# Kernel tuning notes

Measured on AMD Instinct MI355X. Metric: run time of the kernel, lower is better.

Reference implementation:

```python
import jax, jax.numpy as jnp
import numpy as np

B, V = 8, 128  # batch, cubic volume side


def setup_inputs() -> dict:
    key = jax.random.key(0)
    k1, k2 = jax.random.split(key)
    input_volume1 = jax.random.normal(k1, (B, V, V, V), dtype=jnp.float32)
    input_volume2 = jax.random.normal(k2, (B, V, V, V), dtype=jnp.float32)
    return {"input_volume1": input_volume1, "input_volume2": input_volume2}


def reference(input_volume1, input_volume2):
    # Full circular 3D cross-correlation over all relative shifts:
    #   out[b, t] = sum_r v1[b, r] * v2[b, (r + t) mod V]  (t, r are 3D indices)
    # computed via the convolution theorem with real FFTs.
    axes = (1, 2, 3)
    f1 = jnp.fft.rfftn(input_volume1, axes=axes)          # [B, V, V, V//2+1] complex
    f2 = jnp.fft.rfftn(input_volume2, axes=axes)
    out = jnp.fft.irfftn(f1 * jnp.conj(f2), s=(V, V, V), axes=axes)
    return out.astype(jnp.float32)
```

## Files before the change

kernel.cpp:

```cpp
#include <hip/hip_runtime.h>
#include <math.h>


#define V    128
#define V2   16384
#define V3   2097152
#define NB   8
#define PR1  134
#define PC1  66
#define P3Q  130
#define PH3  34
#define SLICE (V * PH3)

__device__ __forceinline__ int bitrev7(int x) {
  return (int)(__brev((unsigned)x) >> 25);
}
__device__ __forceinline__ int negrev(int j) {
  int k = bitrev7(j);
  return bitrev7((V - k) & (V - 1));
}

__device__ __forceinline__ float2 cmul(float2 a, float2 b) {
  return make_float2(a.x * b.x - a.y * b.y, a.x * b.y + a.y * b.x);
}
__device__ __forceinline__ float2 cmulc(float2 a, float2 b) {
  return make_float2(a.x * b.x + a.y * b.y, a.y * b.x - a.x * b.y);
}
__device__ __forceinline__ float2 csqr(float2 a) {
  return make_float2(a.x * a.x - a.y * a.y, 2.0f * a.x * a.y);
}
__device__ __forceinline__ float2 f2add(float2 a, float2 b) {
  return make_float2(a.x + b.x, a.y + b.y);
}
__device__ __forceinline__ float2 f2sub(float2 a, float2 b) {
  return make_float2(a.x - b.x, a.y - b.y);
}
__device__ __forceinline__ float2 NI(float2 z) { return make_float2(z.y, -z.x); }
__device__ __forceinline__ float2 PI(float2 z) { return make_float2(-z.y, z.x); }

#define KC1 0.92387953251128675613f
#define KS1 0.38268343236508977173f
#define KR  0.70710678118654752440f

template <int CTRL>
__device__ __forceinline__ float dppf(float v) {
  return __int_as_float(
      __builtin_amdgcn_update_dpp(0, __float_as_int(v), CTRL, 0xF, 0xF, true));
}
template <int CTRL>
__device__ __forceinline__ float2 dpp2(float2 v) {
  return make_float2(dppf<CTRL>(v.x), dppf<CTRL>(v.y));
}

struct WFT {
  float2 w1, w2, w4, w8, ts4, ts2;
  float sg4, sg2, sg1;
  bool up4, up2;
  int e;

  __device__ void init(int lq) {
    e = lq ^ (((lq >> 2) & 1) * 3);
    const float k = -6.28318530717958647692f / 128.0f;
    w1 = make_float2(cosf(k * (float)e), sinf(k * (float)e));
    w2 = csqr(w1);
    w4 = csqr(w2);
    w8 = csqr(w4);
    up4 = (e >> 2) & 1;
    up2 = (e >> 1) & 1;
    const bool up1 = e & 1;
    sg4 = up4 ? -1.0f : 1.0f;
    sg2 = up2 ? -1.0f : 1.0f;
    sg1 = up1 ? -1.0f : 1.0f;
    const int m4 = e & 3;
    float2 w8p = (m4 == 0) ? make_float2(1.0f, 0.0f)
               : (m4 == 1) ? make_float2(KR, -KR)
               : (m4 == 2) ? make_float2(0.0f, -1.0f)
                           : make_float2(-KR, -KR);
    ts4 = up4 ? w8p : make_float2(1.0f, 0.0f);
    ts2 = (up2 && (e & 1)) ? make_float2(0.0f, -1.0f) : make_float2(1.0f, 0.0f);
  }

  __device__ __forceinline__ void xf4(float2* c, int n) const {
#pragma unroll
    for (int j = 0; j < n; ++j) {
      float2 p = dpp2<0x141>(c[j]);
      float2 t = make_float2(fmaf(c[j].x, sg4, p.x), fmaf(c[j].y, sg4, p.y));
      c[j] = cmul(t, ts4);
    }
#pragma unroll
    for (int j = 0; j < n; ++j) {
      float2 p = dpp2<0x4E>(c[j]);
      float2 t = make_float2(fmaf(c[j].x, sg2, p.x), fmaf(c[j].y, sg2, p.y));
      c[j] = cmul(t, ts2);
    }
#pragma unroll
    for (int j = 0; j < n; ++j) {
      float2 p = dpp2<0xB1>(c[j]);
      c[j] = make_float2(fmaf(c[j].x, sg1, p.x), fmaf(c[j].y, sg1, p.y));
    }
  }
  __device__ __forceinline__ void xi4(float2* c, int n) const {
#pragma unroll
    for (int j = 0; j < n; ++j) {
      float2 p = dpp2<0xB1>(c[j]);
      c[j] = make_float2(fmaf(c[j].x, sg1, p.x), fmaf(c[j].y, sg1, p.y));
    }
#pragma unroll
    for (int j = 0; j < n; ++j) {
      float2 m = cmulc(c[j], ts2);
      float2 q = make_float2(up2 ? m.x : c[j].x, up2 ? m.y : c[j].y);
      float2 p = dpp2<0x4E>(q);
      c[j] = make_float2(fmaf(q.x, sg2, p.x), fmaf(q.y, sg2, p.y));
    }
#pragma unroll
    for (int j = 0; j < n; ++j) {
      float2 m = cmulc(c[j], ts4);
      float2 q = make_float2(up4 ? m.x : c[j].x, up4 ? m.y : c[j].y);
      float2 p = dpp2<0x141>(q);
      c[j] = make_float2(fmaf(q.x, sg4, p.x), fmaf(q.y, sg4, p.y));
    }
  }

  __device__ __forceinline__ void fwd128(float2 c[16]) const {
    const float2 tA = cmul(w1, make_float2(KC1, -KS1));
    const float2 tB = cmul(w1, make_float2(KR, -KR));
    const float2 tC = cmul(w1, make_float2(KS1, -KC1));
#pragma unroll
    for (int j = 0; j < 8; ++j) {
      float2 u = c[j], v = c[j + 8];
      c[j] = f2add(u, v);
      const int q = j & 3;
      float2 tw = (q == 0) ? w1 : (q == 1) ? tA : (q == 2) ? tB : tC;
      float2 t = cmul(f2sub(u, v), tw);
      c[j + 8] = (j < 4) ? t : NI(t);
    }
    const float2 t2 = cmul(w2, make_float2(KR, -KR));
#pragma unroll
    for (int g = 0; g < 2; ++g) {
#pragma unroll
      for (int j0 = 0; j0 < 4; ++j0) {
        const int j = g * 8 + j0;
        float2 u = c[j], v = c[j + 4];
        c[j] = f2add(u, v);
        float2 t = cmul(f2sub(u, v), (j0 & 1) ? t2 : w2);
        c[j + 4] = (j0 < 2) ? t : NI(t);
      }
    }
    const float2 w4n = NI(w4);
#pragma unroll
    for (int g = 0; g < 4; ++g) {
#pragma unroll
      for (int j0 = 0; j0 < 2; ++j0) {
        const int j = g * 4 + j0;
        float2 u = c[j], v = c[j + 2];
        c[j] = f2add(u, v);
        c[j + 2] = cmul(f2sub(u, v), j0 ? w4n : w4);
      }
    }
#pragma unroll
    for (int j = 0; j < 16; j += 2) {
      float2 u = c[j], v = c[j + 1];
      c[j] = f2add(u, v);
      c[j + 1] = cmul(f2sub(u, v), w8);
    }
    xf4(c, 16);
  }

  __device__ __forceinline__ void inv128(float2 c[16]) const {
    xi4(c, 16);
#pragma unroll
    for (int j = 0; j < 16; j += 2) {
      float2 m = cmulc(c[j + 1], w8);
      float2 u = c[j];
      c[j] = f2add(u, m);
      c[j + 1] = f2sub(u, m);
    }
#pragma unroll
    for (int g = 0; g < 4; ++g) {
#pragma unroll
      for (int j0 = 0; j0 < 2; ++j0) {
        const int j = g * 4 + j0;
        float2 m0 = cmulc(c[j + 2], w4);
        float2 m = j0 ? PI(m0) : m0;
        float2 u = c[j];
        c[j] = f2add(u, m);
        c[j + 2] = f2sub(u, m);
      }
    }
    const float2 t2 = cmul(w2, make_float2(KR, -KR));
#pragma unroll
    for (int g = 0; g < 2; ++g) {
#pragma unroll
      for (int j0 = 0; j0 < 4; ++j0) {
        const int j = g * 8 + j0;
        float2 m0 = cmulc(c[j + 4], (j0 & 1) ? t2 : w2);
        float2 m = (j0 < 2) ? m0 : PI(m0);
        float2 u = c[j];
        c[j] = f2add(u, m);
        c[j + 4] = f2sub(u, m);
      }
    }
    const float2 tA = cmul(w1, make_float2(KC1, -KS1));
    const float2 tB = cmul(w1, make_float2(KR, -KR));
    const float2 tC = cmul(w1, make_float2(KS1, -KC1));
#pragma unroll
    for (int j = 0; j < 8; ++j) {
      const int q = j & 3;
      float2 tw = (q == 0) ? w1 : (q == 1) ? tA : (q == 2) ? tB : tC;
      float2 m0 = cmulc(c[j + 8], tw);
      float2 m = (j < 4) ? m0 : PI(m0);
      float2 u = c[j];
      c[j] = f2add(u, m);
      c[j + 8] = f2sub(u, m);
    }
  }

  __device__ __forceinline__ void fwd64(float2 c[8]) const {
    const float2 t2 = cmul(w2, make_float2(KR, -KR));
#pragma unroll
    for (int j = 0; j < 4; ++j) {
      float2 u = c[j], v = c[j + 4];
      c[j] = f2add(u, v);
      float2 t = cmul(f2sub(u, v), (j & 1) ? t2 : w2);
      c[j + 4] = (j < 2) ? t : NI(t);
    }
    const float2 w4n = NI(w4);
#pragma unroll
    for (int g = 0; g < 2; ++g) {
#pragma unroll
      for (int j0 = 0; j0 < 2; ++j0) {
        const int j = g * 4 + j0;
        float2 u = c[j], v = c[j + 2];
        c[j] = f2add(u, v);
        c[j + 2] = cmul(f2sub(u, v), j0 ? w4n : w4);
      }
    }
#pragma unroll
    for (int j = 0; j < 8; j += 2) {
      float2 u = c[j], v = c[j + 1];
      c[j] = f2add(u, v);
      c[j + 1] = cmul(f2sub(u, v), w8);
    }
    xf4(c, 8);
  }
};

__global__ __launch_bounds__(512) void k_fwd_xy(const float* __restrict__ v1,
                                                const float* __restrict__ v2,
                                                float2* __restrict__ Z) {
  __shared__ float2 s[64 * PR1];
  const int tid = threadIdx.x, lane = tid & 63, wave = tid >> 6;
  const int g = tid >> 3, lq = tid & 7;
  const int bz = blockIdx.x >> 1, h = blockIdx.x & 1;
  const int b = bz >> 7, z1 = bz & 127;
  WFT F;
  F.init(lq);
  const int e = F.e;
  const size_t pb = (size_t)b * V3 + (size_t)z1 * V2;
  if (h == 0) {
#pragma unroll
    for (int it = 0; it < 4; ++it) {
      const int idx = tid + it * 512;
      const int r = idx >> 5, x = (idx & 31) << 2;
      const float* p1 = v1 + pb + (size_t)r * V + x;
      const float* p2 = v2 + pb + (size_t)r * V + x;
      const float4 a  = *(const float4*)p1;
      const float4 ab = *(const float4*)(p1 + 64 * V);
      const float4 q  = *(const float4*)p2;
      const float4 qb = *(const float4*)(p2 + 64 * V);
      float2* dst = s + r * PR1 + x;
      float4 w0 = make_float4(a.x + ab.x, q.x + qb.x, a.y + ab.y, q.y + qb.y);
      float4 w1v = make_float4(a.z + ab.z, q.z + qb.z, a.w + ab.w, q.w + qb.w);
      *(float4*)(dst) = w0;
      *(float4*)(dst + 2) = w1v;
    }
  } else {
    const float kk = -6.28318530717958647692f / 128.0f;
#pragma unroll
    for (int it = 0; it < 4; ++it) {
      const int idx = tid + it * 512;
      const int r = idx >> 5, x = (idx & 31) << 2;
      const float2 Wr = make_float2(cosf(kk * (float)r), sinf(kk * (float)r));
      const float* p1 = v1 + pb + (size_t)r * V + x;
      const float* p2 = v2 + pb + (size_t)r * V + x;
      const float4 a  = *(const float4*)p1;
      const float4 ab = *(const float4*)(p1 + 64 * V);
      const float4 q  = *(const float4*)p2;
      const float4 qb = *(const float4*)(p2 + 64 * V);
      float2* dst = s + r * PR1 + x;
      const float2 d0 = cmul(make_float2(a.x - ab.x, q.x - qb.x), Wr);
      const float2 d1 = cmul(make_float2(a.y - ab.y, q.y - qb.y), Wr);
      const float2 d2 = cmul(make_float2(a.z - ab.z, q.z - qb.z), Wr);
      const float2 d3 = cmul(make_float2(a.w - ab.w, q.w - qb.w), Wr);
      *(float4*)(dst) = make_float4(d0.x, d0.y, d1.x, d1.y);
      *(float4*)(dst + 2) = make_float4(d2.x, d2.y, d3.x, d3.y);
    }
  }
  __syncthreads();
  float2 c[16];
#pragma unroll
  for (int j = 0; j < 16; ++j) c[j] = s[g * PR1 + e + 8 * j];
  F.fwd128(c);
#pragma unroll
  for (int j = 0; j < 16; ++j) s[g * PR1 + e + 8 * j] = c[j];
  __syncthreads();
  float2 ca[8], cb[8];
#pragma unroll
  for (int j = 0; j < 8; ++j) {
    const int r = e + 8 * j;
    ca[j] = s[r * PR1 + g];
    cb[j] = s[r * PR1 + g + 64];
  }
  __syncthreads();
  F.fwd64(ca);
  F.fwd64(cb);
#pragma unroll
  for (int j = 0; j < 8; ++j) {
    s[g * PC1 + e + 8 * j] = ca[j];
    s[(g + 64) * PC1 + e + 8 * j] = cb[j];
  }
  __syncthreads();
  {
    const int l2 = (lane & 31) << 1;
    for (int L = wave * 2 + (lane >> 5); L < 128; L += 16) {
      const size_t zb = ((size_t)(b * V + L) * V + z1) * V + h * 64;
      *(float4*)&Z[zb + l2] = *(const float4*)&s[L * PC1 + l2];
    }
  }
}

__global__ __launch_bounds__(512) void k_z_fused(float2* __restrict__ Z) {
  __shared__ float2 T[2 * SLICE];
  const int tid = threadIdx.x, lane = tid & 63, wave = tid >> 6;
  const int o = lane >> 3, lq = lane & 7;
  const int blk = blockIdx.x;
  const int b = blk >> 8, idx = blk & 255;
  int x0, x1, jb0, jb1;
  bool within = false;
  {
    const int h = idx >> 7, r2 = idx & 127;
    if (r2 < 126) {
      const int k = (r2 >> 1) + 1, cc = r2 & 1;
      const int xa = bitrev7(k), xb = bitrev7(V - k);
      if (h == 0) { x0 = xa; x1 = xb; jb0 = cc * 32; jb1 = cc * 32; }
      else { x0 = cc ? xb : xa; x1 = cc ? xa : xb; jb0 = 64; jb1 = 96; }
    } else {
      x0 = x1 = r2 - 126;
      if (h == 0) { jb0 = 0; jb1 = 32; within = true; }
      else { jb0 = 64; jb1 = 96; }
    }
  }
  WFT F;
  F.init(lq);
  const int e = F.e;
  const size_t base0 = (size_t)(b * V + x0) * V2 + jb0;
  const size_t base1 = (size_t)(b * V + x1) * V2 + jb1;

  for (int p = tid; p < 2048; p += 512) {
    const int z = p >> 4, w = (p & 15) << 1;
    *(float4*)&T[z * PH3 + w] = *(const float4*)&Z[base0 + (size_t)z * V + w];
  }
  for (int p = tid; p < 2048; p += 512) {
    const int z = p >> 4, w = (p & 15) << 1;
    *(float4*)&T[SLICE + z * PH3 + w] =
        *(const float4*)&Z[base1 + (size_t)z * V + w];
  }
  __syncthreads();

  const int col = wave * 8 + o;
  const int tb = (col >> 5) * SLICE, yc = col & 31;
  float2 c[16];
#pragma unroll
  for (int j = 0; j < 16; ++j) c[j] = T[tb + (e + 8 * j) * PH3 + yc];
  F.fwd128(c);
#pragma unroll
  for (int j = 0; j < 16; ++j) T[tb + (e + 8 * j) * PH3 + yc] = c[j];
  __syncthreads();

  if (!within) {
    for (int p = tid; p < 4096; p += 512) {
      const int z = p >> 5, t = p & 31;
      const int zm = negrev(z), tm = negrev(jb0 + t) & 31;
      const float2 a  = T[z * PH3 + t];
      const float2 bb = T[SLICE + zm * PH3 + tm];
      const float f1r = 0.5f * (a.x + bb.x), f1i = 0.5f * (a.y - bb.y);
      const float f2r = 0.5f * (a.y + bb.y), f2i = 0.5f * (bb.x - a.x);
      const float gr = f1r * f2r + f1i * f2i;
      const float gi = f1i * f2r - f1r * f2i;
      T[z * PH3 + t] = make_float2(gr, gi);
      T[SLICE + zm * PH3 + tm] = make_float2(gr, -gi);
    }
  } else {
    for (int p = tid; p < 8192; p += 512) {
      const int s2 = p >> 12, z = (p >> 5) & 127, t = p & 31;
      const int zm = negrev(z), tm = negrev(s2 * 32 + t) & 31;
      const int pl = z * 32 + t, pm = zm * 32 + tm;
      if (pm < pl) continue;
      const float2 a  = T[s2 * SLICE + z * PH3 + t];
      const float2 bb = T[s2 * SLICE + zm * PH3 + tm];
      const float f1r = 0.5f * (a.x + bb.x), f1i = 0.5f * (a.y - bb.y);
      const float f2r = 0.5f * (a.y + bb.y), f2i = 0.5f * (bb.x - a.x);
      const float gr = f1r * f2r + f1i * f2i;
      const float gi = f1i * f2r - f1r * f2i;
      T[s2 * SLICE + z * PH3 + t] = make_float2(gr, gi);
      if (pm != pl) T[s2 * SLICE + zm * PH3 + tm] = make_float2(gr, -gi);
    }
  }
  __syncthreads();

#pragma unroll
  for (int j = 0; j < 16; ++j) c[j] = T[tb + (e + 8 * j) * PH3 + yc];
  F.inv128(c);
#pragma unroll
  for (int j = 0; j < 16; ++j) T[tb + (e + 8 * j) * PH3 + yc] = c[j];
  __syncthreads();

  for (int p = tid; p < 2048; p += 512) {
    const int z = p >> 4, w = (p & 15) << 1;
    *(float4*)&Z[base0 + (size_t)z * V + w] = *(const float4*)&T[z * PH3 + w];
  }
  for (int p = tid; p < 2048; p += 512) {
    const int z = p >> 4, w = (p & 15) << 1;
    *(float4*)&Z[base1 + (size_t)z * V + w] =
        *(const float4*)&T[SLICE + z * PH3 + w];
  }
}

__global__ __launch_bounds__(512) void k_inv_xy(const float2* __restrict__ Z,
                                                float* __restrict__ out) {
  __shared__ float2 s[64 * P3Q];
  const int tid = threadIdx.x, lane = tid & 63, wave = tid >> 6;
  const int g = tid >> 3, lq = tid & 7;
  const int r8 = blockIdx.x & 7, hp = (blockIdx.x >> 3) & 1;
  const int unit = (blockIdx.x >> 4) * 8 + r8;
  const int b = unit >> 7, z1 = unit & 127;
  WFT F;
  F.init(lq);
  const int e = F.e;
  float2 c[16];
#pragma unroll 1
  for (int half = 0; half < 2; ++half) {
    const int x = g + 64 * half;
    const size_t zb = ((size_t)(b * V + x) * V + z1) * V;
#pragma unroll
    for (int j = 0; j < 16; ++j) c[j] = Z[zb + e + 8 * j];
    F.inv128(c);
    if (hp == 0) {
#pragma unroll
      for (int jj = 0; jj < 8; ++jj) s[(e + 8 * jj) * P3Q + x] = c[jj];
    } else {
#pragma unroll
      for (int jj = 0; jj < 8; ++jj) s[(e + 8 * jj) * P3Q + x] = c[jj + 8];
    }
  }
  __syncthreads();
  const float sc = 1.0f / 2097152.0f;
  {
#pragma unroll
    for (int j = 0; j < 16; ++j) c[j] = s[g * P3Q + e + 8 * j];
    F.inv128(c);
    float* fr = (float*)(s + g * P3Q);
#pragma unroll
    for (int j = 0; j < 16; ++j) fr[e + 8 * j] = c[j].x * sc;
  }
  __syncthreads();
  {
    const int col = (lane & 31) << 2;
    for (int r2 = wave; r2 < 32; r2 += 8) {
      const int row = 2 * r2 + (lane >> 5);
      const size_t gg =
          (size_t)b * V3 + (size_t)z1 * V2 + (size_t)(hp * 64 + row) * V;
      *(float4*)&out[gg + col] =
          *(const float4*)((const float*)(s + row * P3Q) + col);
    }
  }
}

extern "C" void kernel_launch(void* const* d_in, const int* in_sizes, int n_in,
                              void* d_out, int out_size, void* d_ws, size_t ws_size,
                              hipStream_t stream) {
  const float* v1 = (const float*)d_in[0];
  const float* v2 = (const float*)d_in[1];
  float* out = (float*)d_out;
  float2* Z  = (float2*)d_ws;

  k_fwd_xy<<<NB * V * 2, 512, 0, stream>>>(v1, v2, Z);
  k_z_fused<<<NB * 256, 512, 0, stream>>>(Z);
  k_inv_xy<<<NB * V * 2, 512, 0, stream>>>(Z, out);
}
```

Measured before the change: 307.9 us.

## Exploit Hermitian symmetry to skip redundant inverse z-FFTs and reload input rows

```diff
diff --git a/kernel.cpp b/kernel.cpp
--- a/kernel.cpp
+++ b/kernel.cpp
@@ -257,43 +257,42 @@
   F.init(lq);
   const int e = F.e;
   const size_t pb = (size_t)b * V3 + (size_t)z1 * V2;
-  if (h == 0) {
-#pragma unroll
-    for (int it = 0; it < 4; ++it) {
-      const int idx = tid + it * 512;
-      const int r = idx >> 5, x = (idx & 31) << 2;
-      const float* p1 = v1 + pb + (size_t)r * V + x;
-      const float* p2 = v2 + pb + (size_t)r * V + x;
-      const float4 a  = *(const float4*)p1;
-      const float4 ab = *(const float4*)(p1 + 64 * V);
-      const float4 q  = *(const float4*)p2;
-      const float4 qb = *(const float4*)(p2 + 64 * V);
-      float2* dst = s + r * PR1 + x;
-      float4 w0 = make_float4(a.x + ab.x, q.x + qb.x, a.y + ab.y, q.y + qb.y);
-      float4 w1v = make_float4(a.z + ab.z, q.z + qb.z, a.w + ab.w, q.w + qb.w);
-      *(float4*)(dst) = w0;
-      *(float4*)(dst + 2) = w1v;
-    }
-  } else {
-    const float kk = -6.28318530717958647692f / 128.0f;
-#pragma unroll
-    for (int it = 0; it < 4; ++it) {
-      const int idx = tid + it * 512;
-      const int r = idx >> 5, x = (idx & 31) << 2;
+  {
+    const int r = tid >> 3;
+    const float* p1r = v1 + pb + (size_t)r * V;
+    const float* p2r = v2 + pb + (size_t)r * V;
+    if (h == 0) {
+#pragma unroll
+      for (int it = 0; it < 4; ++it) {
+        const int x = ((tid & 7) + 8 * it) << 2;
+        const float4 a  = *(const float4*)(p1r + x);
+        const float4 ab = *(const float4*)(p1r + x + 64 * V);
+        const float4 q  = *(const float4*)(p2r + x);
+        const float4 qb = *(const float4*)(p2r + x + 64 * V);
+        float2* dst = s + r * PR1 + x;
+        *(float4*)(dst) =
+            make_float4(a.x + ab.x, q.x + qb.x, a.y + ab.y, q.y + qb.y);
+        *(float4*)(dst + 2) =
+            make_float4(a.z + ab.z, q.z + qb.z, a.w + ab.w, q.w + qb.w);
+      }
+    } else {
+      const float kk = -6.28318530717958647692f / 128.0f;
       const float2 Wr = make_float2(cosf(kk * (float)r), sinf(kk * (float)r));
-      const float* p1 = v1 + pb + (size_t)r * V + x;
-      const float* p2 = v2 + pb + (size_t)r * V + x;
-      const float4 a  = *(const float4*)p1;
-      const float4 ab = *(const float4*)(p1 + 64 * V);
-      const float4 q  = *(const float4*)p2;
-      const float4 qb = *(const float4*)(p2 + 64 * V);
-      float2* dst = s + r * PR1 + x;
-      const float2 d0 = cmul(make_float2(a.x - ab.x, q.x - qb.x), Wr);
-      const float2 d1 = cmul(make_float2(a.y - ab.y, q.y - qb.y), Wr);
-      const float2 d2 = cmul(make_float2(a.z - ab.z, q.z - qb.z), Wr);
-      const float2 d3 = cmul(make_float2(a.w - ab.w, q.w - qb.w), Wr);
-      *(float4*)(dst) = make_float4(d0.x, d0.y, d1.x, d1.y);
-      *(float4*)(dst + 2) = make_float4(d2.x, d2.y, d3.x, d3.y);
+#pragma unroll
+      for (int it = 0; it < 4; ++it) {
+        const int x = ((tid & 7) + 8 * it) << 2;
+        const float4 a  = *(const float4*)(p1r + x);
+        const float4 ab = *(const float4*)(p1r + x + 64 * V);
+        const float4 q  = *(const float4*)(p2r + x);
+        const float4 qb = *(const float4*)(p2r + x + 64 * V);
+        float2* dst = s + r * PR1 + x;
+        const float2 d0 = cmul(make_float2(a.x - ab.x, q.x - qb.x), Wr);
+        const float2 d1 = cmul(make_float2(a.y - ab.y, q.y - qb.y), Wr);
+        const float2 d2 = cmul(make_float2(a.z - ab.z, q.z - qb.z), Wr);
+        const float2 d3 = cmul(make_float2(a.w - ab.w, q.w - qb.w), Wr);
+        *(float4*)(dst) = make_float4(d0.x, d0.y, d1.x, d1.y);
+        *(float4*)(dst + 2) = make_float4(d2.x, d2.y, d3.x, d3.y);
+      }
     }
   }
   __syncthreads();
@@ -350,6 +349,9 @@
       else { jb0 = 64; jb1 = 96; }
     }
   }
+  const bool crossAB = (x0 != x1);
+  const bool keep0 = !crossAB || (bitrev7(x0) <= 64);
+  const bool keep1 = !crossAB || !keep0;
   WFT F;
   F.init(lq);
   const int e = F.e;
@@ -408,21 +410,30 @@
   }
   __syncthreads();
 
-#pragma unroll
-  for (int j = 0; j < 16; ++j) c[j] = T[tb + (e + 8 * j) * PH3 + yc];
-  F.inv128(c);
-#pragma unroll
-  for (int j = 0; j < 16; ++j) T[tb + (e + 8 * j) * PH3 + yc] = c[j];
-  __syncthreads();
-
-  for (int p = tid; p < 2048; p += 512) {
-    const int z = p >> 4, w = (p & 15) << 1;
-    *(float4*)&Z[base0 + (size_t)z * V + w] = *(const float4*)&T[z * PH3 + w];
-  }
-  for (int p = tid; p < 2048; p += 512) {
-    const int z = p >> 4, w = (p & 15) << 1;
-    *(float4*)&Z[base1 + (size_t)z * V + w] =
-        *(const float4*)&T[SLICE + z * PH3 + w];
+  {
+    const bool act = (col < 32) ? keep0 : keep1;
+    if (act) {
+#pragma unroll
+      for (int j = 0; j < 16; ++j) c[j] = T[tb + (e + 8 * j) * PH3 + yc];
+      F.inv128(c);
+#pragma unroll
+      for (int j = 0; j < 16; ++j) T[tb + (e + 8 * j) * PH3 + yc] = c[j];
+    }
+  }
+  __syncthreads();
+
+  if (keep0) {
+    for (int p = tid; p < 2048; p += 512) {
+      const int z = p >> 4, w = (p & 15) << 1;
+      *(float4*)&Z[base0 + (size_t)z * V + w] = *(const float4*)&T[z * PH3 + w];
+    }
+  }
+  if (keep1) {
+    for (int p = tid; p < 2048; p += 512) {
+      const int z = p >> 4, w = (p & 15) << 1;
+      *(float4*)&Z[base1 + (size_t)z * V + w] =
+          *(const float4*)&T[SLICE + z * PH3 + w];
+    }
   }
 }
 
@@ -441,16 +452,21 @@
 #pragma unroll 1
   for (int half = 0; half < 2; ++half) {
     const int x = g + 64 * half;
-    const size_t zb = ((size_t)(b * V + x) * V + z1) * V;
+    const bool isA = (bitrev7(x) <= 64);
+    const int xs = isA ? x : negrev(x);
+    const float sgn = isA ? 1.0f : -1.0f;
+    const size_t zb = ((size_t)(b * V + xs) * V + z1) * V;
 #pragma unroll
     for (int j = 0; j < 16; ++j) c[j] = Z[zb + e + 8 * j];
     F.inv128(c);
     if (hp == 0) {
 #pragma unroll
-      for (int jj = 0; jj < 8; ++jj) s[(e + 8 * jj) * P3Q + x] = c[jj];
+      for (int jj = 0; jj < 8; ++jj)
+        s[(e + 8 * jj) * P3Q + x] = make_float2(c[jj].x, c[jj].y * sgn);
     } else {
 #pragma unroll
-      for (int jj = 0; jj < 8; ++jj) s[(e + 8 * jj) * P3Q + x] = c[jj + 8];
+      for (int jj = 0; jj < 8; ++jj)
+        s[(e + 8 * jj) * P3Q + x] = make_float2(c[jj + 8].x, c[jj + 8].y * sgn);
     }
   }
   __syncthreads();
```

After: 309.2 us. About the same (+0.4%).
